# Kernel optimization log

Hardware: AMD Instinct MI355X
Metric: run time of the kernel (lower is better)

The kernel has to match this reference:

```python
import jax, jax.numpy as jnp
import numpy as np

H = 4
N = 50000
D_IN = 128
D_MODEL = 256
NCLASS = 40
B_S = 1
BH = B_S * H
LN_EPS = 1e-5


def sparse_perm_1D(indices, values, feats, n, bh):
    """Batched sparse (bh,n,n) @ dense (bh,n,d): gather -> scale -> segment-sum scatter."""
    gathered = feats[indices[0], indices[2]]              # (nnz, d)
    contrib = values[:, None] * gathered                   # (nnz, d)
    seg = indices[0] * n + indices[1]                      # (nnz,)
    out = jax.ops.segment_sum(contrib, seg, num_segments=bh * n)
    return out.reshape(bh, n, -1)


def layer_norm(x, gamma, beta):
    mu = jnp.mean(x, axis=-1, keepdims=True)
    var = jnp.var(x, axis=-1, keepdims=True)
    return (x - mu) * jax.lax.rsqrt(var + LN_EPS) * gamma + beta


def setup_inputs() -> dict:
    key = jax.random.key(0)
    k1, k2, k3, k4, k5, k6, k7 = jax.random.split(key, 7)
    # per-(batch*head) permutation sigma: nonzero at (b, i, sigma_b(i))
    perm_keys = jax.random.split(k1, BH)
    sigma = jax.vmap(lambda k: jax.random.permutation(k, N))(perm_keys)  # (BH, N)
    b_idx = jnp.repeat(jnp.arange(BH), N)
    row_idx = jnp.tile(jnp.arange(N), BH)
    col_idx = sigma.reshape(-1)
    perm_indices = jnp.stack([b_idx, row_idx, col_idx], axis=0).astype(jnp.int32)  # (3, BH*N)
    perm_values = jax.random.uniform(k2, (BH * N,), dtype=jnp.float32)
    features = jax.random.normal(k3, (B_S, N, D_IN), dtype=jnp.float32)
    appd = jax.random.normal(k4, (B_S, N, D_IN), dtype=jnp.float32)
    # parameters
    w_scale_in = 1.0 / np.sqrt(2 * D_IN)
    W_in = jax.random.uniform(k5, (2 * D_IN, D_MODEL), dtype=jnp.float32, minval=-w_scale_in, maxval=w_scale_in)
    b_in = jnp.zeros((D_MODEL,), dtype=jnp.float32)
    ln_gamma = jnp.ones((D_MODEL * H,), dtype=jnp.float32)
    ln_beta = jnp.zeros((D_MODEL * H,), dtype=jnp.float32)
    w_scale_h = 1.0 / np.sqrt(D_MODEL * H)
    W_head = jax.random.uniform(k6, (D_MODEL * H, NCLASS), dtype=jnp.float32, minval=-w_scale_h, maxval=w_scale_h)
    b_head = jax.random.uniform(k7, (NCLASS,), dtype=jnp.float32, minval=-w_scale_h, maxval=w_scale_h)
    return {"perm_indices": perm_indices, "perm_values": perm_values,
            "features": features, "appd": appd,
            "W_in": W_in, "b_in": b_in,
            "ln_gamma": ln_gamma, "ln_beta": ln_beta,
            "W_head": W_head, "b_head": b_head}


def reference(perm_indices, perm_values, features, appd, W_in, b_in, ln_gamma, ln_beta, W_head, b_head):
    # concat auxiliary features, replicate per head: (B_S,N,2*D_IN) -> (BH,N,2*D_IN)
    feat = jnp.concatenate([features, appd], axis=-1)
    feat = jnp.broadcast_to(feat[:, None], (B_S, H, N, 2 * D_IN)).reshape(BH, N, 2 * D_IN)
    # permute rows: perm @ feat
    x = sparse_perm_1D(perm_indices, perm_values, feat, N, BH)
    # ff_in + relu (dropout is identity at eval)
    x = jax.nn.relu(x @ W_in + b_in)                       # (BH, N, D_MODEL)
    # nlayers == nblocks == 0: compress/uncompress loops are empty
    # inverse permutation: perm^T @ x (swap row/col indices)
    idx_t = jnp.stack([perm_indices[0], perm_indices[2], perm_indices[1]], axis=0)
    y = sparse_perm_1D(idx_t, perm_values, x, N, BH)       # (BH, N, D_MODEL)
    # (B_S,H,N,D) -> (B_S,N,H*D)
    y = y.reshape(B_S, H, N, D_MODEL).transpose(0, 2, 1, 3).reshape(B_S, N, H * D_MODEL)
    y = layer_norm(y, ln_gamma, ln_beta)
    return y @ W_head + b_head                             # (B_S, N, NCLASS)
```

## Files before the change

### kernel.cpp

```cpp
#include <hip/hip_runtime.h>
#include <hip/hip_bf16.h>

#define NROW 50000
#define DIN 128
#define DM 256
#define HH 4
#define NC 40
#define BHN 200000
#define NBLK 3125

typedef float f32x4 __attribute__((ext_vector_type(4)));
typedef short bf16x8 __attribute__((ext_vector_type(8)));

__device__ __forceinline__ unsigned int pk2(float lo, float hi) {
    __hip_bfloat162 h = __float22bfloat162_rn(make_float2(lo, hi));
    return *(unsigned int*)&h;
}

__global__ __launch_bounds__(256) void k_prep(const int* __restrict__ pi,
                                              const float* __restrict__ pv,
                                              const float* __restrict__ Win,
                                              const float* __restrict__ Wh,
                                              const float* __restrict__ gamma,
                                              const float* __restrict__ beta,
                                              const float* __restrict__ bh,
                                              float* __restrict__ vcol,
                                              unsigned short* __restrict__ Wpk,
                                              unsigned short* __restrict__ Wgpk,
                                              float* __restrict__ bias2,
                                              float* __restrict__ wsum) {
    const int bid = blockIdx.x, tid = threadIdx.x;
    if (bid < 196) {
        int k4 = (bid * 256 + tid) * 4;
        if (k4 < BHN) {
            int4   c4 = *(const int4*)&pi[2 * BHN + k4];
            float4 v4 = *(const float4*)&pv[k4];
            int b = (k4 >= 150000) ? 3 : (k4 >= 100000) ? 2 : (k4 >= 50000) ? 1 : 0;
            float* vb = vcol + b * NROW;
            vb[c4.x] = v4.x; vb[c4.y] = v4.y; vb[c4.z] = v4.z; vb[c4.w] = v4.w;
        }
    } else if (bid < 212) {
        int base = (bid - 196) * 512;
        #pragma unroll
        for (int qq = 0; qq < 2; ++qq) {
            int s = base + qq * 256 + tid;
            int ln = s & 63;
            int t  = (s >> 6) & 15;
            int kc = s >> 10;
            int n  = t * 16 + (ln & 15);
            int kb = kc * 32 + ((ln >> 4) << 3);
            union { unsigned int ui[4]; uint4 v4; } u;
            #pragma unroll
            for (int jj = 0; jj < 4; ++jj)
                u.ui[jj] = pk2(Win[(kb + 2 * jj) * DM + n], Win[(kb + 2 * jj + 1) * DM + n]);
            *(uint4*)&Wpk[s * 8] = u.v4;
        }
    } else if (bid < 224) {
        int base = (bid - 212) * 512;
        #pragma unroll
        for (int qq = 0; qq < 2; ++qq) {
            int s = base + qq * 256 + tid;
            int ln = s & 63;
            int u6 = s >> 6;
            int t  = u6 % 3;
            int v6 = u6 / 3;
            int kc = v6 & 7;
            int h  = v6 >> 3;
            int c  = t * 16 + (ln & 15);
            int dbase = h * 256 + kc * 32 + ((ln >> 4) << 2);
            union { unsigned int ui[4]; uint4 v4; } u;
            if (c < NC) {
                #pragma unroll
                for (int jj = 0; jj < 4; ++jj) {
                    int dA = dbase + ((jj >> 1) << 4) + ((jj & 1) << 1);
                    u.ui[jj] = pk2(gamma[dA] * Wh[dA * NC + c],
                                   gamma[dA + 1] * Wh[(dA + 1) * NC + c]);
                }
            } else {
                u.v4 = make_uint4(0u, 0u, 0u, 0u);
            }
            *(uint4*)&Wgpk[s * 8] = u.v4;
        }
    } else {
        __shared__ float redb[256], redw[256];
        int c = bid - 224;
        float sb = 0.f, sw = 0.f;
        #pragma unroll
        for (int q = 0; q < 4; ++q) {
            int d = tid + 256 * q;
            float w = Wh[d * NC + c];
            sb = fmaf(beta[d], w, sb);
            sw = fmaf(gamma[d], w, sw);
        }
        redb[tid] = sb; redw[tid] = sw;
        __syncthreads();
        for (int st = 128; st > 0; st >>= 1) {
            if (tid < st) { redb[tid] += redb[tid + st]; redw[tid] += redw[tid + st]; }
            __syncthreads();
        }
        if (tid == 0) { bias2[c] = bh[c] + redb[0]; wsum[c] = redw[0]; }
    }
}

#define Y_PASS(H, HALF) { \
    const float vh = vm[H]; \
    _Pragma("unroll") \
    for (int tt = 0; tt < 8; ++tt) { \
        float4 b4 = *(const float4*)&bshm[((HALF) * 8 + tt) * 16 + quad * 4]; \
        float y0 = vh * fmaxf(fmaf(vh, accG[tt][0], b4.x), 0.f); \
        float y1 = vh * fmaxf(fmaf(vh, accG[tt][1], b4.y), 0.f); \
        float y2 = vh * fmaxf(fmaf(vh, accG[tt][2], b4.z), 0.f); \
        float y3 = vh * fmaxf(fmaf(vh, accG[tt][3], b4.w), 0.f); \
        s_ += (y0 + y1) + (y2 + y3); \
        ss_ = fmaf(y0, y0, ss_); ss_ = fmaf(y1, y1, ss_); \
        ss_ = fmaf(y2, y2, ss_); ss_ = fmaf(y3, y3, ss_); \
        ya[tt * 2]     = pk2(y0, y1); \
        ya[tt * 2 + 1] = pk2(y2, y3); \
    } }

__global__ __launch_bounds__(64, 3) void k_fused(
    const float* __restrict__ feats, const float* __restrict__ appd,
    const unsigned short* __restrict__ Wpk,
    const unsigned short* __restrict__ Wgpk,
    const float* __restrict__ vcol,
    const float* __restrict__ b_in,
    const float* __restrict__ bias2,
    const float* __restrict__ wsum,
    float* __restrict__ out)
{
    __shared__ __align__(16) float bshm[256];

    const int tid = threadIdx.x;
    const int ln = tid;
    const int quad = ln >> 4;
    const int lr = ln & 15;
    const int jw = blockIdx.x * 16;
    const int ar = min(jw + lr, NROW - 1);

    #pragma unroll
    for (int q = 0; q < 4; ++q) bshm[tid + 64 * q] = b_in[tid + 64 * q];
    __syncthreads();

    float vm[HH];
    #pragma unroll
    for (int h = 0; h < HH; ++h) vm[h] = vcol[h * NROW + ar];

    const unsigned short* wpL = Wpk  + (size_t)ln * 8;
    const unsigned short* wgL = Wgpk + (size_t)ln * 8;

    const f32x4 zero4 = {0.f, 0.f, 0.f, 0.f};
    float s_ = 0.f, ss_ = 0.f;
    f32x4 accO[3];
    #pragma unroll
    for (int t = 0; t < 3; ++t) accO[t] = zero4;
    f32x4 accG[8];
    unsigned int ya[16];

    #pragma unroll
    for (int half = 0; half < 2; ++half) {
        if (half == 1) asm volatile("" ::: "memory");

        unsigned int afr[8][4];
        {
            const float* rf = feats + (size_t)ar * DIN;
            const float* ra = appd  + (size_t)ar * DIN;
            #pragma unroll
            for (int kc = 0; kc < 8; ++kc) {
                const float* src = (kc < 4) ? rf : ra;
                const int ko = (kc & 3) * 32 + quad * 8;
                float4 x0 = *(const float4*)(src + ko);
                float4 x1 = *(const float4*)(src + ko + 4);
                afr[kc][0] = pk2(x0.x, x0.y);
                afr[kc][1] = pk2(x0.z, x0.w);
                afr[kc][2] = pk2(x1.x, x1.y);
                afr[kc][3] = pk2(x1.z, x1.w);
            }
        }

        #pragma unroll
        for (int kc = 0; kc < 8; ++kc) {
            asm volatile("" ::: "memory");
            bf16x8 wf[8];
            #pragma unroll
            for (int th = 0; th < 8; ++th)
                wf[th] = *(const bf16x8*)&wpL[(size_t)(kc * 16 + half * 8 + th) * 512];
            union { unsigned int ui[4]; bf16x8 v; } a;
            a.ui[0] = afr[kc][0]; a.ui[1] = afr[kc][1];
            a.ui[2] = afr[kc][2]; a.ui[3] = afr[kc][3];
            #pragma unroll
            for (int th = 0; th < 8; ++th)
                accG[th] = __builtin_amdgcn_mfma_f32_16x16x32_bf16(
                    wf[th], a.v, (kc == 0) ? zero4 : accG[th], 0, 0, 0);
        }

        #pragma unroll
        for (int h = 0; h < HH; ++h) {
            asm volatile("" ::: "memory");
            bf16x8 wg[12];
            #pragma unroll
            for (int kcr = 0; kcr < 2; ++kcr)
                #pragma unroll
                for (int t3 = 0; t3 < 3; ++t3)
                    wg[kcr * 3 + t3] = *(const bf16x8*)
                        &wgL[(size_t)(((h * 8 + half * 4 + kcr) * 3 + t3)) * 512];
            Y_PASS(h, half)
            #pragma unroll
            for (int kcr = 2; kcr < 4; ++kcr)
                #pragma unroll
                for (int t3 = 0; t3 < 3; ++t3)
                    wg[kcr * 3 + t3] = *(const bf16x8*)
                        &wgL[(size_t)(((h * 8 + half * 4 + kcr) * 3 + t3)) * 512];
            #pragma unroll
            for (int kcr = 0; kcr < 4; ++kcr) {
                union { unsigned int ui[4]; bf16x8 v; } af;
                af.ui[0] = ya[4 * kcr];     af.ui[1] = ya[4 * kcr + 1];
                af.ui[2] = ya[4 * kcr + 2]; af.ui[3] = ya[4 * kcr + 3];
                #pragma unroll
                for (int t3 = 0; t3 < 3; ++t3)
                    accO[t3] = __builtin_amdgcn_mfma_f32_16x16x32_bf16(
                        af.v, wg[kcr * 3 + t3], accO[t3], 0, 0, 0);
            }
        }
    }

    s_  += __shfl_xor(s_, 16);  s_  += __shfl_xor(s_, 32);
    ss_ += __shfl_xor(ss_, 16); ss_ += __shfl_xor(ss_, 32);
    float mm  = s_ * (1.f / 1024.f);
    float var = ss_ * (1.f / 1024.f) - mm * mm;
    float rs  = rsqrtf(var + 1e-5f);
    float nm  = -mm * rs;

    float rs_r[4], nm_r[4];
    #pragma unroll
    for (int rg = 0; rg < 4; ++rg) {
        int rloc = quad * 4 + rg;
        rs_r[rg] = __shfl(rs, rloc);
        nm_r[rg] = __shfl(nm, rloc);
    }
    #pragma unroll
    for (int t = 0; t < 3; ++t) {
        int c = t * 16 + lr;
        if (c < NC) {
            float w2 = wsum[c], b2 = bias2[c];
            #pragma unroll
            for (int rg = 0; rg < 4; ++rg) {
                int row = jw + quad * 4 + rg;
                if (row < NROW)
                    out[(size_t)row * NC + c] = fmaf(rs_r[rg], accO[t][rg], fmaf(nm_r[rg], w2, b2));
            }
        }
    }
}

extern "C" void kernel_launch(void* const* d_in, const int* in_sizes, int n_in,
                              void* d_out, int out_size, void* d_ws, size_t ws_size,
                              hipStream_t stream) {
    const int*   pi    = (const int*)d_in[0];
    const float* pv    = (const float*)d_in[1];
    const float* feats = (const float*)d_in[2];
    const float* appd  = (const float*)d_in[3];
    const float* Win   = (const float*)d_in[4];
    const float* b_in  = (const float*)d_in[5];
    const float* gamma = (const float*)d_in[6];
    const float* beta  = (const float*)d_in[7];
    const float* Wh    = (const float*)d_in[8];
    const float* bh    = (const float*)d_in[9];
    float* out = (float*)d_out;

    char* w = (char*)d_ws;
    float*          vcolW  = (float*)w;
    unsigned short* WpkW   = (unsigned short*)(w + 800000);
    unsigned short* WgpkW  = (unsigned short*)(w + 931072);
    float*          bias2W = (float*)(w + 1029376);
    float*          wsumW  = (float*)(w + 1029536);

    k_prep<<<264, 256, 0, stream>>>(pi, pv, Win, Wh, gamma, beta, bh,
                                    vcolW, WpkW, WgpkW, bias2W, wsumW);
    k_fused<<<NBLK, 64, 0, stream>>>(feats, appd, WpkW, WgpkW, vcolW, b_in,
                                     bias2W, wsumW, out);
}
```

Measured before the change: 149.2 us.

## Process two 16-row tiles per wavefront to reuse weight fragments

Each 64-thread block now handles 32 rows as two 16-row tiles. Every weight fragment loaded for the input projection and the head projection feeds MFMAs for both tiles, which halves weight-load traffic per row and gives independent MFMA chains to interleave. The grid size is halved and the occupancy hint drops from 3 to 2 waves per SIMD because accumulator and register use roughly doubles, so there is a risk of spills or less latency hiding.

New measurement: 141.2 us. 5.4% less time.

```diff
diff --git a/kernel.cpp b/kernel.cpp
--- a/kernel.cpp
+++ b/kernel.cpp
@@ -7,7 +7,7 @@
 #define HH 4
 #define NC 40
 #define BHN 200000
-#define NBLK 3125
+#define NBLK 1563
 
 typedef float f32x4 __attribute__((ext_vector_type(4)));
 typedef short bf16x8 __attribute__((ext_vector_type(8)));
@@ -102,23 +102,49 @@
     }
 }
 
-#define Y_PASS(H, HALF) { \
-    const float vh = vm[H]; \
+#define Y_PASS(VH, ACC, S, SS, HALF) { \
     _Pragma("unroll") \
     for (int tt = 0; tt < 8; ++tt) { \
         float4 b4 = *(const float4*)&bshm[((HALF) * 8 + tt) * 16 + quad * 4]; \
-        float y0 = vh * fmaxf(fmaf(vh, accG[tt][0], b4.x), 0.f); \
-        float y1 = vh * fmaxf(fmaf(vh, accG[tt][1], b4.y), 0.f); \
-        float y2 = vh * fmaxf(fmaf(vh, accG[tt][2], b4.z), 0.f); \
-        float y3 = vh * fmaxf(fmaf(vh, accG[tt][3], b4.w), 0.f); \
-        s_ += (y0 + y1) + (y2 + y3); \
-        ss_ = fmaf(y0, y0, ss_); ss_ = fmaf(y1, y1, ss_); \
-        ss_ = fmaf(y2, y2, ss_); ss_ = fmaf(y3, y3, ss_); \
+        float y0 = (VH) * fmaxf(fmaf((VH), ACC[tt][0], b4.x), 0.f); \
+        float y1 = (VH) * fmaxf(fmaf((VH), ACC[tt][1], b4.y), 0.f); \
+        float y2 = (VH) * fmaxf(fmaf((VH), ACC[tt][2], b4.z), 0.f); \
+        float y3 = (VH) * fmaxf(fmaf((VH), ACC[tt][3], b4.w), 0.f); \
+        S += (y0 + y1) + (y2 + y3); \
+        SS = fmaf(y0, y0, SS); SS = fmaf(y1, y1, SS); \
+        SS = fmaf(y2, y2, SS); SS = fmaf(y3, y3, SS); \
         ya[tt * 2]     = pk2(y0, y1); \
         ya[tt * 2 + 1] = pk2(y2, y3); \
     } }
 
-__global__ __launch_bounds__(64, 3) void k_fused(
+#define HEAD_MFMA(ACCO) { \
+    _Pragma("unroll") \
+    for (int kcr = 0; kcr < 4; ++kcr) { \
+        union { unsigned int ui[4]; bf16x8 v; } af; \
+        af.ui[0] = ya[4 * kcr];     af.ui[1] = ya[4 * kcr + 1]; \
+        af.ui[2] = ya[4 * kcr + 2]; af.ui[3] = ya[4 * kcr + 3]; \
+        _Pragma("unroll") \
+        for (int t3 = 0; t3 < 3; ++t3) \
+            ACCO[t3] = __builtin_amdgcn_mfma_f32_16x16x32_bf16( \
+                af.v, wg[kcr * 3 + t3], ACCO[t3], 0, 0, 0); \
+    } }
+
+#define AFR_PACK(AFR, AR) { \
+    const float* rf = feats + (size_t)(AR) * DIN; \
+    const float* ra = appd  + (size_t)(AR) * DIN; \
+    _Pragma("unroll") \
+    for (int kc = 0; kc < 8; ++kc) { \
+        const float* src = (kc < 4) ? rf : ra; \
+        const int ko = (kc & 3) * 32 + quad * 8; \
+        float4 x0 = *(const float4*)(src + ko); \
+        float4 x1 = *(const float4*)(src + ko + 4); \
+        AFR[kc][0] = pk2(x0.x, x0.y); \
+        AFR[kc][1] = pk2(x0.z, x0.w); \
+        AFR[kc][2] = pk2(x1.x, x1.y); \
+        AFR[kc][3] = pk2(x1.z, x1.w); \
+    } }
+
+__global__ __launch_bounds__(64, 2) void k_fused(
     const float* __restrict__ feats, const float* __restrict__ appd,
     const unsigned short* __restrict__ Wpk,
     const unsigned short* __restrict__ Wgpk,
@@ -134,48 +160,39 @@
     const int ln = tid;
     const int quad = ln >> 4;
     const int lr = ln & 15;
-    const int jw = blockIdx.x * 16;
-    const int ar = min(jw + lr, NROW - 1);
+    const int jw = blockIdx.x * 32;
+    const int ar0 = min(jw + lr, NROW - 1);
+    const int ar1 = min(jw + 16 + lr, NROW - 1);
 
     #pragma unroll
     for (int q = 0; q < 4; ++q) bshm[tid + 64 * q] = b_in[tid + 64 * q];
     __syncthreads();
 
-    float vm[HH];
-    #pragma unroll
-    for (int h = 0; h < HH; ++h) vm[h] = vcol[h * NROW + ar];
+    float vm0[HH], vm1[HH];
+    #pragma unroll
+    for (int h = 0; h < HH; ++h) {
+        vm0[h] = vcol[h * NROW + ar0];
+        vm1[h] = vcol[h * NROW + ar1];
+    }
 
     const unsigned short* wpL = Wpk  + (size_t)ln * 8;
     const unsigned short* wgL = Wgpk + (size_t)ln * 8;
 
     const f32x4 zero4 = {0.f, 0.f, 0.f, 0.f};
-    float s_ = 0.f, ss_ = 0.f;
-    f32x4 accO[3];
-    #pragma unroll
-    for (int t = 0; t < 3; ++t) accO[t] = zero4;
-    f32x4 accG[8];
+    float s0 = 0.f, ss0 = 0.f, s1 = 0.f, ss1 = 0.f;
+    f32x4 accO0[3], accO1[3];
+    #pragma unroll
+    for (int t = 0; t < 3; ++t) { accO0[t] = zero4; accO1[t] = zero4; }
+    f32x4 accG0[8], accG1[8];
     unsigned int ya[16];
 
     #pragma unroll
     for (int half = 0; half < 2; ++half) {
         if (half == 1) asm volatile("" ::: "memory");
 
-        unsigned int afr[8][4];
-        {
-            const float* rf = feats + (size_t)ar * DIN;
-            const float* ra = appd  + (size_t)ar * DIN;
-            #pragma unroll
-            for (int kc = 0; kc < 8; ++kc) {
-                const float* src = (kc < 4) ? rf : ra;
-                const int ko = (kc & 3) * 32 + quad * 8;
-                float4 x0 = *(const float4*)(src + ko);
-                float4 x1 = *(const float4*)(src + ko + 4);
-                afr[kc][0] = pk2(x0.x, x0.y);
-                afr[kc][1] = pk2(x0.z, x0.w);
-                afr[kc][2] = pk2(x1.x, x1.y);
-                afr[kc][3] = pk2(x1.z, x1.w);
-            }
-        }
+        unsigned int afr0[8][4], afr1[8][4];
+        AFR_PACK(afr0, ar0)
+        AFR_PACK(afr1, ar1)
 
         #pragma unroll
         for (int kc = 0; kc < 8; ++kc) {
@@ -184,13 +201,18 @@
             #pragma unroll
             for (int th = 0; th < 8; ++th)
                 wf[th] = *(const bf16x8*)&wpL[(size_t)(kc * 16 + half * 8 + th) * 512];
-            union { unsigned int ui[4]; bf16x8 v; } a;
-            a.ui[0] = afr[kc][0]; a.ui[1] = afr[kc][1];
-            a.ui[2] = afr[kc][2]; a.ui[3] = afr[kc][3];
-            #pragma unroll
-            for (int th = 0; th < 8; ++th)
-                accG[th] = __builtin_amdgcn_mfma_f32_16x16x32_bf16(
-                    wf[th], a.v, (kc == 0) ? zero4 : accG[th], 0, 0, 0);
+            union { unsigned int ui[4]; bf16x8 v; } a0, a1;
+            a0.ui[0] = afr0[kc][0]; a0.ui[1] = afr0[kc][1];
+            a0.ui[2] = afr0[kc][2]; a0.ui[3] = afr0[kc][3];
+            a1.ui[0] = afr1[kc][0]; a1.ui[1] = afr1[kc][1];
+            a1.ui[2] = afr1[kc][2]; a1.ui[3] = afr1[kc][3];
+            #pragma unroll
+            for (int th = 0; th < 8; ++th) {
+                accG0[th] = __builtin_amdgcn_mfma_f32_16x16x32_bf16(
+                    wf[th], a0.v, (kc == 0) ? zero4 : accG0[th], 0, 0, 0);
+                accG1[th] = __builtin_amdgcn_mfma_f32_16x16x32_bf16(
+                    wf[th], a1.v, (kc == 0) ? zero4 : accG1[th], 0, 0, 0);
+            }
         }
 
         #pragma unroll
@@ -203,39 +225,38 @@
                 for (int t3 = 0; t3 < 3; ++t3)
                     wg[kcr * 3 + t3] = *(const bf16x8*)
                         &wgL[(size_t)(((h * 8 + half * 4 + kcr) * 3 + t3)) * 512];
-            Y_PASS(h, half)
+            Y_PASS(vm0[h], accG0, s0, ss0, half)
             #pragma unroll
             for (int kcr = 2; kcr < 4; ++kcr)
                 #pragma unroll
                 for (int t3 = 0; t3 < 3; ++t3)
                     wg[kcr * 3 + t3] = *(const bf16x8*)
                         &wgL[(size_t)(((h * 8 + half * 4 + kcr) * 3 + t3)) * 512];
-            #pragma unroll
-            for (int kcr = 0; kcr < 4; ++kcr) {
-                union { unsigned int ui[4]; bf16x8 v; } af;
-                af.ui[0] = ya[4 * kcr];     af.ui[1] = ya[4 * kcr + 1];
-                af.ui[2] = ya[4 * kcr + 2]; af.ui[3] = ya[4 * kcr + 3];
-                #pragma unroll
-                for (int t3 = 0; t3 < 3; ++t3)
-                    accO[t3] = __builtin_amdgcn_mfma_f32_16x16x32_bf16(
-                        af.v, wg[kcr * 3 + t3], accO[t3], 0, 0, 0);
-            }
-        }
-    }
-
-    s_  += __shfl_xor(s_, 16);  s_  += __shfl_xor(s_, 32);
-    ss_ += __shfl_xor(ss_, 16); ss_ += __shfl_xor(ss_, 32);
-    float mm  = s_ * (1.f / 1024.f);
-    float var = ss_ * (1.f / 1024.f) - mm * mm;
-    float rs  = rsqrtf(var + 1e-5f);
-    float nm  = -mm * rs;
-
-    float rs_r[4], nm_r[4];
+            HEAD_MFMA(accO0)
+            Y_PASS(vm1[h], accG1, s1, ss1, half)
+            HEAD_MFMA(accO1)
+        }
+    }
+
+    s0  += __shfl_xor(s0, 16);  s0  += __shfl_xor(s0, 32);
+    ss0 += __shfl_xor(ss0, 16); ss0 += __shfl_xor(ss0, 32);
+    s1  += __shfl_xor(s1, 16);  s1  += __shfl_xor(s1, 32);
+    ss1 += __shfl_xor(ss1, 16); ss1 += __shfl_xor(ss1, 32);
+    float mm0  = s0 * (1.f / 1024.f);
+    float rs0  = rsqrtf(ss0 * (1.f / 1024.f) - mm0 * mm0 + 1e-5f);
+    float nm0  = -mm0 * rs0;
+    float mm1  = s1 * (1.f / 1024.f);
+    float rs1  = rsqrtf(ss1 * (1.f / 1024.f) - mm1 * mm1 + 1e-5f);
+    float nm1  = -mm1 * rs1;
+
+    float rs_r0[4], nm_r0[4], rs_r1[4], nm_r1[4];
     #pragma unroll
     for (int rg = 0; rg < 4; ++rg) {
         int rloc = quad * 4 + rg;
-        rs_r[rg] = __shfl(rs, rloc);
-        nm_r[rg] = __shfl(nm, rloc);
+        rs_r0[rg] = __shfl(rs0, rloc);
+        nm_r0[rg] = __shfl(nm0, rloc);
+        rs_r1[rg] = __shfl(rs1, rloc);
+        nm_r1[rg] = __shfl(nm1, rloc);
     }
     #pragma unroll
     for (int t = 0; t < 3; ++t) {
@@ -244,9 +265,12 @@
             float w2 = wsum[c], b2 = bias2[c];
             #pragma unroll
             for (int rg = 0; rg < 4; ++rg) {
-                int row = jw + quad * 4 + rg;
-                if (row < NROW)
-                    out[(size_t)row * NC + c] = fmaf(rs_r[rg], accO[t][rg], fmaf(nm_r[rg], w2, b2));
+                int row0 = jw + quad * 4 + rg;
+                int row1 = row0 + 16;
+                if (row0 < NROW)
+                    out[(size_t)row0 * NC + c] = fmaf(rs_r0[rg], accO0[t][rg], fmaf(nm_r0[rg], w2, b2));
+                if (row1 < NROW)
+                    out[(size_t)row1 * NC + c] = fmaf(rs_r1[rg], accO1[t][rg], fmaf(nm_r1[rg], w2, b2));
             }
         }
     }
```
